# Performance work log

Measured on AMD Instinct MI355X. Metric: run time of the kernel, lower is better.

Reference implementation:

```python
import jax, jax.numpy as jnp
import numpy as np


def _conv1x1(x, w, b):
    # x: [B,C,H,W], w: [O,C], b: [O] -> [B,O,H,W]
    return jnp.einsum('bchw,oc->bohw', x, w) + b[None, :, None, None]


def setup_inputs() -> dict:
    key = jax.random.key(0)
    ks = jax.random.split(key, 5)
    B, C, H, W = 4, 256, 64, 64
    C2 = C // 2
    scale = 0.02  # keep attention logits in a sane range
    return {
        'x': jax.random.normal(ks[0], (B, C, H, W), dtype=jnp.float32),
        'w_theta': jax.random.normal(ks[1], (C2, C), dtype=jnp.float32) * scale,
        'b_theta': jnp.zeros((C2,), dtype=jnp.float32),
        'w_phi': jax.random.normal(ks[2], (C2, C), dtype=jnp.float32) * scale,
        'b_phi': jnp.zeros((C2,), dtype=jnp.float32),
        'w_g': jax.random.normal(ks[3], (C2, C), dtype=jnp.float32) * scale,
        'b_g': jnp.zeros((C2,), dtype=jnp.float32),
        'w_out': jax.random.normal(ks[4], (C, C2), dtype=jnp.float32) * scale,
        'b_out': jnp.zeros((C,), dtype=jnp.float32),
    }


def reference(x, w_theta, b_theta, w_phi, b_phi, w_g, b_g, w_out, b_out):
    B, C, H, W = x.shape
    C2 = C // 2
    N = H * W
    theta = _conv1x1(x, w_theta, b_theta).reshape(B, C2, N)  # [B,C2,N]
    phi = _conv1x1(x, w_phi, b_phi).reshape(B, C2, N)        # [B,C2,N]
    g = _conv1x1(x, w_g, b_g).reshape(B, C2, N)              # [B,C2,N]
    # non-local attention: scores[b,m,n] = theta[b,:,m] . phi[b,:,n]
    scores = jnp.einsum('bcm,bcn->bmn', theta, phi)          # [B,N,N]
    attn = jax.nn.softmax(scores, axis=-1)                   # [B,N,N]
    # output = g @ attn^T : out[b,c,m] = sum_n g[b,c,n] * attn[b,m,n]
    out = jnp.einsum('bcn,bmn->bcm', g, attn)                # [B,C2,N]
    out = out.reshape(B, C2, H, W)
    return x + _conv1x1(out, w_out, b_out)
```

## Files before the change

### kernel.cpp

```cpp
#include <hip/hip_runtime.h>
#include <hip/hip_bf16.h>

#define B_  4
#define C_  256
#define C2_ 128
#define N_  4096
#define LOG2E 1.4426950408889634f

typedef unsigned short u16;
typedef __attribute__((ext_vector_type(8))) short bf16x8;
typedef __attribute__((ext_vector_type(4))) float f32x4;
typedef __attribute__((ext_vector_type(16))) float f32x16;
typedef __attribute__((ext_vector_type(4))) unsigned u32x4;

static __device__ __forceinline__ u16 f2bf(float f) {
    return __builtin_bit_cast(u16, __float2bfloat16(f));
}
static __device__ __forceinline__ float bf2f(u16 u) {
    return __bfloat162float(__builtin_bit_cast(__hip_bfloat16, u));
}
static __device__ __forceinline__ bf16x8 cvt8(const float* p) {
    u16 t[8];
#pragma unroll
    for (int j = 0; j < 8; ++j) t[j] = f2bf(p[j]);
    return *(const bf16x8*)t;
}

#define XW 264

__global__ __launch_bounds__(256, 2) void projx_kernel(
    const float* __restrict__ x,
    const float* __restrict__ wt, const float* __restrict__ wp,
    const float* __restrict__ wg,
    const float* __restrict__ b_theta, const float* __restrict__ b_phi,
    const float* __restrict__ b_g,
    u16* __restrict__ Q, u16* __restrict__ K, u16* __restrict__ V) {
    __shared__ __align__(16) u16 XTs[64][XW];
    __shared__ __align__(16) u16 Ws[64][XW];
    u16 (*Vt)[72] = (u16(*)[72])XTs;

    int p = blockIdx.x;
    int b = (p & 7) >> 1;
    int j = ((p >> 3) << 1) | (p & 1);
    int h  = j >> 6;
    int n0 = (j & 63) * 64;
    int tid = threadIdx.x;
    int wave = tid >> 6, lane = tid & 63, quad = (lane >> 4) & 3, l16 = lane & 15;

#pragma unroll
    for (int it = 0; it < 8; ++it) {
        int idx = it * 256 + tid;
        int q = idx & 15, pp = idx >> 4;
        const float* r0 = x + ((size_t)b * C_ + 2 * pp) * N_ + n0 + 4 * q;
        float4 v0 = *(const float4*)r0;
        float4 v1 = *(const float4*)(r0 + N_);
        const float* f0 = (const float*)&v0;
        const float* f1 = (const float*)&v1;
#pragma unroll
        for (int jj = 0; jj < 4; ++jj) {
            unsigned pk = (unsigned)f2bf(f0[jj]) | ((unsigned)f2bf(f1[jj]) << 16);
            *(unsigned*)&XTs[4 * q + jj][2 * pp] = pk;
        }
    }
    __syncthreads();

    bf16x8 af[8];
#pragma unroll
    for (int ks = 0; ks < 8; ++ks)
        af[ks] = *(const bf16x8*)&XTs[wave * 16 + l16][ks * 32 + quad * 8];
    __syncthreads();

    const float* wms[3]    = { wt, wp, wg };
    const float* biases[3] = { b_theta, b_phi, b_g };

#pragma unroll
    for (int mat = 0; mat < 3; ++mat) {
        const float* wm = wms[mat];
        const float* bias = biases[mat];
#pragma unroll
        for (int it = 0; it < 8; ++it) {
            int idx = it * 256 + tid;
            int row = idx >> 5, c8 = (idx & 31) * 8;
            const float* src = wm + (size_t)(h * 64 + row) * C_ + c8;
            float w8[8];
            *(float4*)&w8[0] = *(const float4*)src;
            *(float4*)&w8[4] = *(const float4*)(src + 4);
            *(bf16x8*)&Ws[row][c8] = cvt8(w8);
        }
        __syncthreads();

        f32x4 acc[4];
#pragma unroll
        for (int i = 0; i < 4; ++i) acc[i] = (f32x4){0.f, 0.f, 0.f, 0.f};
#pragma unroll
        for (int ct = 0; ct < 4; ++ct)
#pragma unroll
            for (int ks = 0; ks < 8; ++ks) {
                bf16x8 bf = *(const bf16x8*)&Ws[ct * 16 + l16][ks * 32 + quad * 8];
                acc[ct] = __builtin_amdgcn_mfma_f32_16x16x32_bf16(
                    af[ks], bf, acc[ct], 0, 0, 0);
            }

        if (mat < 2) {
            u16* dst = mat == 0 ? Q : K;
            float scl = mat == 0 ? LOG2E : 1.0f;
#pragma unroll
            for (int ct = 0; ct < 4; ++ct) {
                int c2 = h * 64 + ct * 16 + l16;
                float bb = bias[c2];
#pragma unroll
                for (int r = 0; r < 4; ++r) {
                    int n = n0 + wave * 16 + quad * 4 + r;
                    dst[((size_t)b * N_ + n) * C2_ + c2] =
                        f2bf((acc[ct][r] + bb) * scl);
                }
            }
        } else {
#pragma unroll
            for (int ct = 0; ct < 4; ++ct) {
                int c2l = ct * 16 + l16;
                float bb = bias[h * 64 + c2l];
#pragma unroll
                for (int r = 0; r < 4; ++r)
                    Vt[c2l][wave * 16 + quad * 4 + r] = f2bf(acc[ct][r] + bb);
            }
        }
        __syncthreads();
    }

#pragma unroll
    for (int it = 0; it < 2; ++it) {
        int idx = it * 256 + tid;
        int row = idx >> 3, n8 = (idx & 7) * 8;
        *(uint4*)(V + ((size_t)b * C2_ + h * 64 + row) * N_ + n0 + n8) =
            *(const uint4*)&Vt[row][n8];
    }
}

__global__ __launch_bounds__(256, 2) void attn_kernel(
    const u16* __restrict__ Q, const u16* __restrict__ K,
    const u16* __restrict__ V, u16* __restrict__ AO,
    u16* __restrict__ Opb, float* __restrict__ lsum, int nsplit) {
    const int BM = 128, BN = 64, D = C2_;
    int p = blockIdx.x;
    int b = (p & 7) >> 1;
    int j = ((p >> 3) << 1) | (p & 1);
    int s  = j >> 5;
    int m0 = (j & 31) * BM;
    int tid  = threadIdx.x;
    int wave = tid >> 6, lane = tid & 63;
    int l32 = lane & 31, hi8 = (lane >> 5) * 8, hi4 = (lane >> 5) * 4;

    __shared__ __align__(16) u16 smem[17920];
    u16 (*Ks)[136] = (u16(*)[136])smem;
    u16 (*Vs)[72]  = (u16(*)[72])(smem + 8704);
    u16* obw = smem + wave * 4352;

    bf16x8 qf[8];
    {
        const u16* qp = Q + ((size_t)b * N_ + m0 + wave * 32 + l32) * D + hi8;
#pragma unroll
        for (int c = 0; c < 8; ++c)
            qf[c] = *(const bf16x8*)(qp + c * 16);
    }

    float l_r = 0.f;
    f32x16 o_acc[4];
#pragma unroll
    for (int i = 0; i < 4; ++i)
#pragma unroll
        for (int r = 0; r < 16; ++r) o_acc[i][r] = 0.f;

    const int tiles = N_ / BN;
    const int base = tiles / nsplit, rem = tiles % nsplit;
    const int t0 = s * base + (s < rem ? s : rem);
    const int cnt = base + (s < rem ? 1 : 0);
    const int nt0 = t0 * BN, nt1 = (t0 + cnt) * BN;

    for (int nt = nt0; nt < nt1; nt += BN) {
        const u16* kp = K + ((size_t)b * N_ + nt) * D;
#pragma unroll
        for (int it = 0; it < 4; ++it) {
            int idx = it * 256 + tid;
            int row = idx >> 4, col = (idx & 15) * 8;
            *(uint4*)&Ks[row][col] = *(const uint4*)(kp + row * D + col);
        }
#pragma unroll
        for (int it = 0; it < 4; ++it) {
            int idx = it * 256 + tid;
            int row = idx >> 3, col = (idx & 7) * 8;
            uint4 raw = *(const uint4*)(V + ((size_t)b * C2_ + row) * N_ + nt + col);
            int dst = (col & ~15) + ((col & 8) >> 1);
            *(uint2*)&Vs[row][dst]     = make_uint2(raw.x, raw.y);
            *(uint2*)&Vs[row][dst + 8] = make_uint2(raw.z, raw.w);
        }
        __syncthreads();

        f32x16 sc0, sc1;
#pragma unroll
        for (int r = 0; r < 16; ++r) { sc0[r] = 0.f; sc1[r] = 0.f; }
#pragma unroll
        for (int c = 0; c < 8; ++c) {
            bf16x8 kf0 = *(const bf16x8*)&Ks[l32][c * 16 + hi8];
            bf16x8 kf1 = *(const bf16x8*)&Ks[32 + l32][c * 16 + hi8];
            sc0 = __builtin_amdgcn_mfma_f32_32x32x16_bf16(kf0, qf[c], sc0, 0, 0, 0);
            sc1 = __builtin_amdgcn_mfma_f32_32x32x16_bf16(kf1, qf[c], sc1, 0, 0, 0);
        }

        unsigned w0[8], w1[8];
#pragma unroll
        for (int t = 0; t < 8; ++t) {
            float a0 = __builtin_amdgcn_exp2f(sc0[2 * t]);
            float a1 = __builtin_amdgcn_exp2f(sc0[2 * t + 1]);
            float b0 = __builtin_amdgcn_exp2f(sc1[2 * t]);
            float b1 = __builtin_amdgcn_exp2f(sc1[2 * t + 1]);
            l_r += (a0 + a1) + (b0 + b1);
            w0[t] = (unsigned)f2bf(a0) | ((unsigned)f2bf(a1) << 16);
            w1[t] = (unsigned)f2bf(b0) | ((unsigned)f2bf(b1) << 16);
        }
        bf16x8 pf[4];
        pf[0] = __builtin_bit_cast(bf16x8, (u32x4){w0[0], w0[1], w0[2], w0[3]});
        pf[1] = __builtin_bit_cast(bf16x8, (u32x4){w0[4], w0[5], w0[6], w0[7]});
        pf[2] = __builtin_bit_cast(bf16x8, (u32x4){w1[0], w1[1], w1[2], w1[3]});
        pf[3] = __builtin_bit_cast(bf16x8, (u32x4){w1[4], w1[5], w1[6], w1[7]});

#pragma unroll
        for (int c = 0; c < 4; ++c)
#pragma unroll
            for (int dblk = 0; dblk < 4; ++dblk) {
                bf16x8 vf = *(const bf16x8*)&Vs[dblk * 32 + l32][c * 16 + hi8];
                o_acc[dblk] = __builtin_amdgcn_mfma_f32_32x32x16_bf16(
                    vf, pf[c], o_acc[dblk], 0, 0, 0);
            }
        __syncthreads();
    }

    float l_tot = l_r + __shfl_xor(l_r, 32);
    float scale = Opb ? 1.0f : 1.0f / l_tot;

#pragma unroll
    for (int dblk = 0; dblk < 4; ++dblk)
#pragma unroll
        for (int r = 0; r < 16; ++r) {
            int d = dblk * 32 + (r & 3) + 8 * (r >> 2) + hi4;
            obw[l32 * 136 + d] = f2bf(o_acc[dblk][r] * scale);
        }

    int mloc = lane >> 1, half = lane & 1;
    if (Opb) {
        size_t row = (size_t)s * (B_ * N_) + (size_t)b * N_ + m0 + wave * 32 + mloc;
#pragma unroll
        for (int k = 0; k < 8; ++k)
            *(uint4*)(Opb + row * C2_ + half * 64 + k * 8) =
                *(const uint4*)&obw[mloc * 136 + half * 64 + k * 8];
        if (lane < 32)
            lsum[(size_t)s * (B_ * N_) + (size_t)b * N_ + m0 + wave * 32 + lane] = l_tot;
    } else {
        size_t row = (size_t)b * N_ + m0 + wave * 32 + mloc;
#pragma unroll
        for (int k = 0; k < 8; ++k)
            *(uint4*)(AO + row * C2_ + half * 64 + k * 8) =
                *(const uint4*)&obw[mloc * 136 + half * 64 + k * 8];
    }
}

#define OW 136

__global__ __launch_bounds__(256, 4) void outproj_kernel(
    const float* __restrict__ x, const u16* __restrict__ Opb,
    const float* __restrict__ lsum, const u16* __restrict__ AO,
    const float* __restrict__ w_out, const float* __restrict__ b_out,
    float* __restrict__ y, int nsplit) {
    __shared__ __align__(16) u16 As[64][OW];
    __shared__ __align__(16) u16 Ws2[64][OW];
    __shared__ float Ls[64];
    float (*Yt)[68] = (float(*)[68])&As[0][0];

    int p = blockIdx.x;
    int b = (p & 7) >> 1;
    int j = ((p >> 3) << 1) | (p & 1);
    int c0 = (j >> 6) * 64;
    int n0 = (j & 63) * 64;
    int tid = threadIdx.x;
    int wave = tid >> 6, lane = tid & 63, quad = (lane >> 4) & 3, l16 = lane & 15;

#pragma unroll
    for (int it = 0; it < 4; ++it) {
        int idx = it * 256 + tid;
        int row = idx >> 4, c8 = (idx & 15) * 8;
        const float* src = w_out + (size_t)(c0 + row) * C2_ + c8;
        float w8[8];
        *(float4*)&w8[0] = *(const float4*)src;
        *(float4*)&w8[4] = *(const float4*)(src + 4);
        *(bf16x8*)&Ws2[row][c8] = cvt8(w8);
    }

    if (nsplit > 1) {
        if (tid < 64) {
            float L = 0.f;
            for (int s = 0; s < nsplit; ++s)
                L += lsum[(size_t)s * (B_ * N_) + (size_t)b * N_ + n0 + tid];
            Ls[tid] = 1.f / L;
        }
        __syncthreads();
#pragma unroll
        for (int it = 0; it < 4; ++it) {
            int idx = it * 256 + tid;
            int n = idx >> 4, c8 = (idx & 15) * 8;
            float a[8] = {0.f, 0.f, 0.f, 0.f, 0.f, 0.f, 0.f, 0.f};
            for (int s = 0; s < nsplit; ++s) {
                const u16* op = Opb +
                    ((size_t)s * (B_ * N_) + (size_t)b * N_ + n0 + n) * C2_ + c8;
                uint4 raw = *(const uint4*)op;
                const u16* rp = (const u16*)&raw;
#pragma unroll
                for (int jj = 0; jj < 8; ++jj) a[jj] += bf2f(rp[jj]);
            }
            float inv = Ls[n];
            u16 o[8];
#pragma unroll
            for (int jj = 0; jj < 8; ++jj) o[jj] = f2bf(a[jj] * inv);
            *(uint4*)&As[n][c8] = *(const uint4*)o;
        }
    } else {
#pragma unroll
        for (int it = 0; it < 4; ++it) {
            int idx = it * 256 + tid;
            int n = idx >> 4, c8 = (idx & 15) * 8;
            *(uint4*)&As[n][c8] =
                *(const uint4*)(AO + ((size_t)b * N_ + n0 + n) * C2_ + c8);
        }
    }
    __syncthreads();

    bf16x8 af[4];
#pragma unroll
    for (int kk = 0; kk < 4; ++kk)
        af[kk] = *(const bf16x8*)&Ws2[wave * 16 + l16][kk * 32 + quad * 8];

    f32x4 acc[4];
#pragma unroll
    for (int i = 0; i < 4; ++i) acc[i] = (f32x4){0.f, 0.f, 0.f, 0.f};

#pragma unroll
    for (int nn = 0; nn < 4; ++nn)
#pragma unroll
        for (int kk = 0; kk < 4; ++kk) {
            bf16x8 bf = *(const bf16x8*)&As[nn * 16 + l16][kk * 32 + quad * 8];
            acc[nn] = __builtin_amdgcn_mfma_f32_16x16x32_bf16(af[kk], bf, acc[nn], 0, 0, 0);
        }

    int cw = c0 + wave * 16;
    float bo[4];
#pragma unroll
    for (int r = 0; r < 4; ++r) bo[r] = b_out[cw + quad * 4 + r];

    __syncthreads();
#pragma unroll
    for (int nn = 0; nn < 4; ++nn)
#pragma unroll
        for (int r = 0; r < 4; ++r)
            Yt[wave * 16 + quad * 4 + r][nn * 16 + l16] = acc[nn][r] + bo[r];
    __syncthreads();

    {
        int row = tid >> 2, sg = (tid & 3) * 16;
        const float4* xr = (const float4*)(x + ((size_t)b * C_ + c0 + row) * N_ + n0 + sg);
        float4*       yr = (float4*)(y + ((size_t)b * C_ + c0 + row) * N_ + n0 + sg);
        const float4* tr = (const float4*)&Yt[row][sg];
#pragma unroll
        for (int jj = 0; jj < 4; ++jj) {
            float4 xv = xr[jj];
            float4 tv = tr[jj];
            yr[jj] = make_float4(xv.x + tv.x, xv.y + tv.y,
                                 xv.z + tv.z, xv.w + tv.w);
        }
    }
}

extern "C" void kernel_launch(void* const* d_in, const int* in_sizes, int n_in,
                              void* d_out, int out_size, void* d_ws, size_t ws_size,
                              hipStream_t stream) {
    const float* x       = (const float*)d_in[0];
    const float* w_theta = (const float*)d_in[1];
    const float* b_theta = (const float*)d_in[2];
    const float* w_phi   = (const float*)d_in[3];
    const float* b_phi   = (const float*)d_in[4];
    const float* w_g     = (const float*)d_in[5];
    const float* b_g     = (const float*)d_in[6];
    const float* w_out   = (const float*)d_in[7];
    const float* b_out   = (const float*)d_in[8];
    float* y = (float*)d_out;

    const size_t SZ = (size_t)B_ * N_ * C2_;
    u16* Q = (u16*)d_ws;
    u16* K = Q + SZ;
    u16* V = K + SZ;
    char* dyn = (char*)(V + SZ);
    size_t fixedB = 3 * SZ * 2;

    size_t perS = SZ * 2 + (size_t)B_ * N_ * 4;

    int S;
    if      (ws_size >= fixedB + 8 * perS) S = 8;
    else if (ws_size >= fixedB + 4 * perS) S = 4;
    else if (ws_size >= fixedB + 2 * perS) S = 2;
    else                                   S = 1;

    u16*   AO  = (u16*)dyn;
    u16*   Opb = nullptr;
    float* ls  = nullptr;
    if (S > 1) {
        Opb = (u16*)dyn;
        ls  = (float*)(Opb + (size_t)S * SZ);
    }

    projx_kernel<<<B_ * (N_ / 64) * 2, 256, 0, stream>>>(
        x, w_theta, w_phi, w_g, b_theta, b_phi, b_g, Q, K, V);
    attn_kernel<<<B_ * (N_ / 128) * S, 256, 0, stream>>>(Q, K, V, AO, Opb, ls, S);
    outproj_kernel<<<B_ * (C_ / 64) * (N_ / 64), 256, 0, stream>>>(
        x, Opb, ls, AO, w_out, b_out, y, S);
}
```

Baseline: 159.7 us.

## Double-buffer K/V tiles in attention kernel and cap KV split at four

Moves the K/V tile loads into a double-buffered shared-memory scheme. The next tile's global loads are issued into registers before the QK MFMAs and written to the alternate buffer before the PV stage, so there is one barrier per iteration instead of two and global latency is hidden behind compute. Shared memory per block doubles to about 70 KB, which may reduce occupancy below the two blocks per CU the launch bounds ask for. The maximum KV split count also drops from 8 to 4, which means fewer blocks and less partial-sum traffic but less parallelism.

```diff
diff --git a/kernel.cpp b/kernel.cpp
--- a/kernel.cpp
+++ b/kernel.cpp
@@ -151,9 +151,7 @@
     int wave = tid >> 6, lane = tid & 63;
     int l32 = lane & 31, hi8 = (lane >> 5) * 8, hi4 = (lane >> 5) * 4;
 
-    __shared__ __align__(16) u16 smem[17920];
-    u16 (*Ks)[136] = (u16(*)[136])smem;
-    u16 (*Vs)[72]  = (u16(*)[72])(smem + 8704);
+    __shared__ __align__(16) u16 smem[35840];
     u16* obw = smem + wave * 4352;
 
     bf16x8 qf[8];
@@ -177,32 +175,58 @@
     const int cnt = base + (s < rem ? 1 : 0);
     const int nt0 = t0 * BN, nt1 = (t0 + cnt) * BN;
 
-    for (int nt = nt0; nt < nt1; nt += BN) {
-        const u16* kp = K + ((size_t)b * N_ + nt) * D;
+    const u16* kbase = K + (size_t)b * N_ * D;
+    const u16* vbase = V + (size_t)b * C2_ * N_;
+
+    int krow = tid >> 4,  kcol = (tid & 15) * 8;
+    int vrow = tid >> 3,  vcol = (tid & 7) * 8;
+    int vdst = (vcol & ~15) + ((vcol & 8) >> 1);
+
+    {
+        uint4 kp4[4], vp4[4];
+#pragma unroll
+        for (int it = 0; it < 4; ++it)
+            kp4[it] = *(const uint4*)(kbase + (size_t)(nt0 + krow + it * 16) * D + kcol);
+#pragma unroll
+        for (int it = 0; it < 4; ++it)
+            vp4[it] = *(const uint4*)(vbase + (size_t)(vrow + it * 32) * N_ + nt0 + vcol);
+#pragma unroll
+        for (int it = 0; it < 4; ++it)
+            *(uint4*)(smem + (krow + it * 16) * 136 + kcol) = kp4[it];
 #pragma unroll
         for (int it = 0; it < 4; ++it) {
-            int idx = it * 256 + tid;
-            int row = idx >> 4, col = (idx & 15) * 8;
-            *(uint4*)&Ks[row][col] = *(const uint4*)(kp + row * D + col);
-        }
-#pragma unroll
-        for (int it = 0; it < 4; ++it) {
-            int idx = it * 256 + tid;
-            int row = idx >> 3, col = (idx & 7) * 8;
-            uint4 raw = *(const uint4*)(V + ((size_t)b * C2_ + row) * N_ + nt + col);
-            int dst = (col & ~15) + ((col & 8) >> 1);
-            *(uint2*)&Vs[row][dst]     = make_uint2(raw.x, raw.y);
-            *(uint2*)&Vs[row][dst + 8] = make_uint2(raw.z, raw.w);
-        }
-        __syncthreads();
+            uint4 raw = vp4[it];
+            u16* vb = smem + 8704 + (vrow + it * 32) * 72;
+            *(uint2*)(vb + vdst)     = make_uint2(raw.x, raw.y);
+            *(uint2*)(vb + vdst + 8) = make_uint2(raw.z, raw.w);
+        }
+    }
+    __syncthreads();
+
+    int cur = 0;
+    for (int i = 0; i < cnt; ++i) {
+        int nt  = nt0 + i * BN;
+        int ntn = (nt + BN < nt1) ? nt + BN : nt;
+        u16* Kc = smem + cur * 17920;
+        u16* Vc = Kc + 8704;
+        u16* Kn = smem + (cur ^ 1) * 17920;
+        u16* Vn = Kn + 8704;
+
+        uint4 kp4[4], vp4[4];
+#pragma unroll
+        for (int it = 0; it < 4; ++it)
+            kp4[it] = *(const uint4*)(kbase + (size_t)(ntn + krow + it * 16) * D + kcol);
+#pragma unroll
+        for (int it = 0; it < 4; ++it)
+            vp4[it] = *(const uint4*)(vbase + (size_t)(vrow + it * 32) * N_ + ntn + vcol);
 
         f32x16 sc0, sc1;
 #pragma unroll
         for (int r = 0; r < 16; ++r) { sc0[r] = 0.f; sc1[r] = 0.f; }
 #pragma unroll
         for (int c = 0; c < 8; ++c) {
-            bf16x8 kf0 = *(const bf16x8*)&Ks[l32][c * 16 + hi8];
-            bf16x8 kf1 = *(const bf16x8*)&Ks[32 + l32][c * 16 + hi8];
+            bf16x8 kf0 = *(const bf16x8*)(Kc + l32 * 136 + c * 16 + hi8);
+            bf16x8 kf1 = *(const bf16x8*)(Kc + (32 + l32) * 136 + c * 16 + hi8);
             sc0 = __builtin_amdgcn_mfma_f32_32x32x16_bf16(kf0, qf[c], sc0, 0, 0, 0);
             sc1 = __builtin_amdgcn_mfma_f32_32x32x16_bf16(kf1, qf[c], sc1, 0, 0, 0);
         }
@@ -225,14 +249,27 @@
         pf[3] = __builtin_bit_cast(bf16x8, (u32x4){w1[4], w1[5], w1[6], w1[7]});
 
 #pragma unroll
+        for (int it = 0; it < 4; ++it)
+            *(uint4*)(Kn + (krow + it * 16) * 136 + kcol) = kp4[it];
+#pragma unroll
+        for (int it = 0; it < 4; ++it) {
+            uint4 raw = vp4[it];
+            u16* vb = Vn + (vrow + it * 32) * 72;
+            *(uint2*)(vb + vdst)     = make_uint2(raw.x, raw.y);
+            *(uint2*)(vb + vdst + 8) = make_uint2(raw.z, raw.w);
+        }
+
+#pragma unroll
         for (int c = 0; c < 4; ++c)
 #pragma unroll
             for (int dblk = 0; dblk < 4; ++dblk) {
-                bf16x8 vf = *(const bf16x8*)&Vs[dblk * 32 + l32][c * 16 + hi8];
+                bf16x8 vf = *(const bf16x8*)(Vc + (dblk * 32 + l32) * 72 + c * 16 + hi8);
                 o_acc[dblk] = __builtin_amdgcn_mfma_f32_32x32x16_bf16(
                     vf, pf[c], o_acc[dblk], 0, 0, 0);
             }
+
         __syncthreads();
+        cur ^= 1;
     }
 
     float l_tot = l_r + __shfl_xor(l_r, 32);
@@ -402,8 +439,7 @@
     size_t perS = SZ * 2 + (size_t)B_ * N_ * 4;
 
     int S;
-    if      (ws_size >= fixedB + 8 * perS) S = 8;
-    else if (ws_size >= fixedB + 4 * perS) S = 4;
+    if      (ws_size >= fixedB + 4 * perS) S = 4;
     else if (ws_size >= fixedB + 2 * perS) S = 2;
     else                                   S = 1;
 
```

Result: faster. 156.5 us (-2.0%).
